# Performance work log

Hardware: AMD Instinct MI355X
Metric: run time of the kernel (lower is better)

## Reference

```python
import jax, jax.numpy as jnp
import numpy as np

E, H, D = 512, 8, 64
B, T = 2, 1024
HD = H * D


def _linear(x, W, b):
    return x @ W + b


def _ln(x, g, b):
    mu = x.mean(-1, keepdims=True)
    var = ((x - mu) ** 2).mean(-1, keepdims=True)
    return (x - mu) / jnp.sqrt(var + 1e-5) * g + b


def _l2norm(x):
    n = jnp.sqrt((x * x).sum(-1, keepdims=True))
    return x / jnp.maximum(n, 1e-12)


def setup_inputs() -> dict:
    key = jax.random.key(0)
    ks = jax.random.split(key, 32)
    s = 0.02
    inp = {
        'x': jax.random.normal(ks[0], (B, T, E), jnp.float32),
        'b_min': jax.random.normal(ks[1], (B, T, E), jnp.float32),
        'b_max': jax.random.normal(ks[2], (B, T, E), jnp.float32),
        'motif_context': jax.random.normal(ks[3], (B, T, E), jnp.float32),
        'Wk': jax.random.normal(ks[4], (E, HD), jnp.float32) * s,
        'bk': jnp.zeros((HD,), jnp.float32),
        'Wq': jax.random.normal(ks[5], (E, HD), jnp.float32) * s,
        'bq': jnp.zeros((HD,), jnp.float32),
        'Wv': jax.random.normal(ks[6], (E, HD), jnp.float32) * s,
        'bv': jnp.zeros((HD,), jnp.float32),
        'Wo': jax.random.normal(ks[7], (HD, E), jnp.float32) * s,
        'bo': jnp.zeros((E,), jnp.float32),
        'Wd': jax.random.normal(ks[8], (E, H), jnp.float32) * s,
        'bd': jnp.zeros((H,), jnp.float32),
        'Wgw': jax.random.normal(ks[9], (E, H), jnp.float32) * s,
        'bgw': jnp.zeros((H,), jnp.float32),
        'Wgf': jax.random.normal(ks[10], (E, H), jnp.float32) * s,
        'bgf': jnp.zeros((H,), jnp.float32),
        'Wps': jax.random.normal(ks[11], (E, E), jnp.float32) * s,
        'bps': jnp.zeros((E,), jnp.float32),
        'ln1_g': jnp.ones((E,), jnp.float32),
        'ln1_b': jnp.zeros((E,), jnp.float32),
        'ln2_g': jnp.ones((E,), jnp.float32),
        'ln2_b': jnp.zeros((E,), jnp.float32),
        'W1': jax.random.normal(ks[12], (E, 4 * E), jnp.float32) * s,
        'b1': jnp.zeros((4 * E,), jnp.float32),
        'W2': jax.random.normal(ks[13], (4 * E, E), jnp.float32) * s,
        'b2': jnp.zeros((E,), jnp.float32),
    }
    return inp


def reference(x, b_min, b_max, motif_context,
              Wk, bk, Wq, bq, Wv, bv, Wo, bo, Wd, bd,
              Wgw, bgw, Wgf, bgf, Wps, bps,
              ln1_g, ln1_b, ln2_g, ln2_b, W1, b1, W2, b2):
    Bs, Ts, Es = x.shape
    x_n = _ln(x, ln1_g, ln1_b)
    k = _l2norm(_linear(x_n, Wk, bk).reshape(Bs, Ts, H, D))
    q = _l2norm(_linear(x_n, Wq, bq).reshape(Bs, Ts, H, D))
    v = jnp.tanh(_linear(x_n, Wv, bv).reshape(Bs, Ts, H, D))
    d = jax.nn.softplus(_linear(x_n, Wd, bd))            # (B,T,H)
    gw = jax.nn.sigmoid(_linear(x_n, Wgw, bgw)) ** 2     # (B,T,H)
    gf = 1.0 - jax.nn.sigmoid(_linear(x_n, Wgf, bgf)) ** 2

    # gated linear recurrent scan via cumsum of rank-1 updates
    v_gated = v * (d * gw)[..., None]                    # (B,T,H,D)
    updates = jnp.einsum('bthi,bthj->bthij', v_gated, k)  # (B,T,H,D,D)
    decay = jnp.clip(d * gf, 1e-6, 0.999)
    log_decay = jnp.log(decay)[..., None, None]          # (B,T,H,1,1)
    exp_cum_decay = jnp.exp(jnp.cumsum(log_decay, axis=1))
    state = jnp.cumsum(updates / (exp_cum_decay + 1e-8), axis=1) * exp_cum_decay
    readout = jnp.einsum('bthij,bthj->bthi', state, q)   # (B,T,H,D)
    next_mem = state[:, -1]

    x2 = x + _linear(readout.reshape(Bs, Ts, HD), Wo, bo) + 0.1 * motif_context
    h = _ln(x2, ln2_g, ln2_b)
    x3 = x2 + _linear(jax.nn.gelu(_linear(h, W1, b1), approximate=False), W2, b2)
    probe = _linear(x3, Wps, bps)
    return (x3, next_mem, b_min + probe, b_max + probe)
```

## Files before the change

### kernel.cpp

```cpp
#include <hip/hip_runtime.h>


typedef unsigned short u16;
typedef unsigned int u32;
typedef __attribute__((ext_vector_type(8))) short short8;
typedef __attribute__((ext_vector_type(4))) float floatx4;

__device__ __forceinline__ float b2f(u16 u) {
  u32 x = ((u32)u) << 16;
  return __uint_as_float(x);
}
__device__ __forceinline__ u16 f2b(float f) {
  u32 x = __float_as_uint(f);
  u32 r = (x + 0x7fffu + ((x >> 16) & 1u)) >> 16;
  return (u16)r;
}
__device__ __forceinline__ float4 b4_to_f4(uint2 u) {
  float4 r;
  r.x = __uint_as_float((u.x & 0xffffu) << 16);
  r.y = __uint_as_float(u.x & 0xffff0000u);
  r.z = __uint_as_float((u.y & 0xffffu) << 16);
  r.w = __uint_as_float(u.y & 0xffff0000u);
  return r;
}

__device__ __forceinline__ void stage16(const u16* g, u16* lds_wave_base) {
  __builtin_amdgcn_global_load_lds((const __attribute__((address_space(1))) void*)g,
                                   (__attribute__((address_space(3))) void*)lds_wave_base,
                                   16, 0, 0);
}

template <int ROWS>
__device__ __forceinline__ void stage_tile(const u16* __restrict__ G, int ldK, int kb,
                                           u16* lds, int tid) {
#pragma unroll
  for (int r = 0; r < ROWS / 64; ++r) {
    int slot = r * 256 + tid;
    int row = slot >> 2;
    int kwg = (slot & 3) ^ ((row >> 1) & 3);
    stage16(G + (size_t)row * ldK + kb * 32 + kwg * 8,
            lds + (size_t)(r * 256 + (tid >> 6) * 64) * 8);
  }
}

__device__ __forceinline__ void ln_row(const float* __restrict__ xr,
                                       const float* __restrict__ g,
                                       const float* __restrict__ bt,
                                       u16* __restrict__ yr, int tid, float* red) {
  float x0 = xr[tid], x1 = xr[tid + 256];
  float s = x0 + x1, ss = x0 * x0 + x1 * x1;
#pragma unroll
  for (int o = 32; o > 0; o >>= 1) { s += __shfl_xor(s, o); ss += __shfl_xor(ss, o); }
  if ((tid & 63) == 0) { red[tid >> 6] = s; red[4 + (tid >> 6)] = ss; }
  __syncthreads();
  float ts = red[0] + red[1] + red[2] + red[3];
  float tss = red[4] + red[5] + red[6] + red[7];
  float mu = ts * (1.f / 512.f);
  float var = tss * (1.f / 512.f) - mu * mu;
  float rstd = 1.0f / sqrtf(var + 1e-5f);
  yr[tid] = f2b((x0 - mu) * rstd * g[tid] + bt[tid]);
  yr[tid + 256] = f2b((x1 - mu) * rstd * g[tid + 256] + bt[tid + 256]);
}

__global__ __launch_bounds__(256) void prep_weights(
    const float* __restrict__ Wk, const float* __restrict__ Wq,
    const float* __restrict__ Wv, const float* __restrict__ Wo,
    const float* __restrict__ Wps, const float* __restrict__ W1,
    const float* __restrict__ W2, const float* __restrict__ Wd,
    const float* __restrict__ Wgw, const float* __restrict__ Wgf,
    const float* __restrict__ bk, const float* __restrict__ bq,
    const float* __restrict__ bv, const float* __restrict__ bd,
    const float* __restrict__ bgw, const float* __restrict__ bgf,
    const float* __restrict__ x, const float* __restrict__ ln1g,
    const float* __restrict__ ln1b,
    u16* __restrict__ WTQ, u16* __restrict__ WTO, u16* __restrict__ WTPS,
    u16* __restrict__ WT1, u16* __restrict__ WT2, float* __restrict__ BQV,
    u16* __restrict__ XN) {
  int bid = blockIdx.x, tid = threadIdx.x;
  __shared__ float tile[32][33];
  __shared__ float red[8];
  if (bid < 3328) {
    const float* src;
    u16* dst;
    int C, rel, tiles_x;
    if (bid < 256)       { src = Wk;  dst = WTQ;           C = 512;  rel = bid;        tiles_x = 16; }
    else if (bid < 512)  { src = Wq;  dst = WTQ + 262144;  C = 512;  rel = bid - 256;  tiles_x = 16; }
    else if (bid < 768)  { src = Wv;  dst = WTQ + 524288;  C = 512;  rel = bid - 512;  tiles_x = 16; }
    else if (bid < 1024) { src = Wo;  dst = WTO;           C = 512;  rel = bid - 768;  tiles_x = 16; }
    else if (bid < 1280) { src = Wps; dst = WTPS;          C = 512;  rel = bid - 1024; tiles_x = 16; }
    else if (bid < 2304) { src = W1;  dst = WT1;           C = 2048; rel = bid - 1280; tiles_x = 64; }
    else                 { src = W2;  dst = WT2;           C = 512;  rel = bid - 2304; tiles_x = 16; }
    int R = (bid >= 1280 && bid < 2304) ? 512 : (bid >= 2304 ? 2048 : 512);
    int c0 = (rel % tiles_x) * 32, r0 = (rel / tiles_x) * 32;
    int tx = tid & 31, ty = tid >> 5;
#pragma unroll
    for (int i = 0; i < 4; ++i)
      tile[ty + i * 8][tx] = src[(size_t)(r0 + ty + i * 8) * C + c0 + tx];
    __syncthreads();
#pragma unroll
    for (int i = 0; i < 4; ++i)
      dst[(size_t)(c0 + ty + i * 8) * R + r0 + tx] = f2b(tile[tx][ty + i * 8]);
  } else if (bid < 3392) {
    int idx = (bid - 3328) * 256 + tid;
    const int stride = 64 * 256;
    for (int i = idx; i < 128 * 512; i += stride) {
      int local = i >> 9, k = i & 511;
      float v = 0.f;
      if (local < 8) v = Wd[k * 8 + local];
      else if (local < 16) v = Wgw[k * 8 + (local - 8)];
      else if (local < 24) v = Wgf[k * 8 + (local - 16)];
      WTQ[(size_t)(1536 + local) * 512 + k] = f2b(v);
    }
    for (int i = idx; i < 1664; i += stride) {
      float v = 0.f;
      if (i < 512) v = bk[i];
      else if (i < 1024) v = bq[i - 512];
      else if (i < 1536) v = bv[i - 1024];
      else if (i < 1544) v = bd[i - 1536];
      else if (i < 1552) v = bgw[i - 1544];
      else if (i < 1560) v = bgf[i - 1552];
      BQV[i] = v;
    }
  } else {
    int row = bid - 3392;
    ln_row(x + (size_t)row * 512, ln1g, ln1b, XN + (size_t)row * 512, tid, red);
  }
}

__global__ __launch_bounds__(256) void ln_f32(const float* __restrict__ X,
                                              const float* __restrict__ g,
                                              const float* __restrict__ bt,
                                              u16* __restrict__ Y) {
  __shared__ float red[8];
  ln_row(X + (size_t)blockIdx.x * 512, g, bt, Y + (size_t)blockIdx.x * 512,
         threadIdx.x, red);
}

template <int EPI>
__global__ __launch_bounds__(256, 4) void gemm64(
    const u16* __restrict__ A, const u16* __restrict__ BT, const float* __restrict__ bias,
    float* __restrict__ outf, float* __restrict__ outf2, u16* __restrict__ outb,
    const float* __restrict__ aux0, const float* __restrict__ aux1, int M, int N, int K) {
  __shared__ __align__(16) u16 As[3][64 * 32];
  __shared__ __align__(16) u16 Bs[3][64 * 32];
  const int tid = threadIdx.x;
  const int lane = tid & 63, wave = tid >> 6;
  const int wm = wave >> 1, wn = wave & 1;
  const int m0 = blockIdx.y * 64, n0 = blockIdx.x * 64;
  floatx4 acc[2][2] = {};
  const int fr = lane & 15, kq = lane >> 4;
  const int nk = K >> 5;
  const u16* Ab = A + (size_t)m0 * K;
  const u16* Bb = BT + (size_t)n0 * K;

  stage_tile<64>(Ab, K, 0, As[0], tid);
  stage_tile<64>(Bb, K, 0, Bs[0], tid);
  if (nk > 1) {
    stage_tile<64>(Ab, K, 1, As[1], tid);
    stage_tile<64>(Bb, K, 1, Bs[1], tid);
  }

  for (int kb = 0; kb < nk; ++kb) {
    const int cur = kb % 3;
    if (kb + 2 < nk) {
      const int nxt = (kb + 2) % 3;
      stage_tile<64>(Ab, K, kb + 2, As[nxt], tid);
      stage_tile<64>(Bb, K, kb + 2, Bs[nxt], tid);
    }
    int ahead = nk - 1 - kb;
    if (ahead > 2) ahead = 2;
    if (ahead == 2) asm volatile("s_waitcnt vmcnt(4)" ::: "memory");
    else if (ahead == 1) asm volatile("s_waitcnt vmcnt(2)" ::: "memory");
    else asm volatile("s_waitcnt vmcnt(0)" ::: "memory");
    asm volatile("s_barrier" ::: "memory");

    short8 af[2], bf[2];
#pragma unroll
    for (int mt = 0; mt < 2; ++mt) {
      int row = wm * 32 + mt * 16 + fr;
      af[mt] = *(const short8*)&As[cur][row * 32 + (kq ^ ((row >> 1) & 3)) * 8];
    }
#pragma unroll
    for (int nt = 0; nt < 2; ++nt) {
      int row = wn * 32 + nt * 16 + fr;
      bf[nt] = *(const short8*)&Bs[cur][row * 32 + (kq ^ ((row >> 1) & 3)) * 8];
    }
#pragma unroll
    for (int mt = 0; mt < 2; ++mt)
#pragma unroll
      for (int nt = 0; nt < 2; ++nt)
        acc[mt][nt] =
            __builtin_amdgcn_mfma_f32_16x16x32_bf16(af[mt], bf[nt], acc[mt][nt], 0, 0, 0);
    asm volatile("s_waitcnt lgkmcnt(0)" ::: "memory");
    asm volatile("s_barrier" ::: "memory");
  }

  const int col = lane & 15;
  const int rbase = (lane >> 4) * 4;
#pragma unroll
  for (int nt = 0; nt < 2; ++nt) {
    int gc = n0 + wn * 32 + nt * 16 + col;
    float bvv = bias[gc];
#pragma unroll
    for (int mt = 0; mt < 2; ++mt) {
      int gr = m0 + wm * 32 + mt * 16 + rbase;
#pragma unroll
      for (int r = 0; r < 4; ++r) {
        size_t idx = (size_t)(gr + r) * N + gc;
        float v = acc[mt][nt][r] + bvv;
        if constexpr (EPI == 0) {
          outf[idx] = v;
        } else if constexpr (EPI == 1) {
          outf[idx] = aux0[idx] + v + 0.1f * aux1[idx];
        } else if constexpr (EPI == 2) {
          outb[idx] = f2b(0.5f * v * (1.f + erff(v * 0.70710678118654752f)));
        } else if constexpr (EPI == 3) {
          float w = aux0[idx] + v;
          outf[idx] = w;
          outb[idx] = f2b(w);
        } else {
          outf[idx] = aux0[idx] + v;
          outf2[idx] = aux1[idx] + v;
        }
      }
    }
  }
}

__global__ __launch_bounds__(512) void post_qkvg(const float* __restrict__ C0,
                                                 u16* __restrict__ KB, u16* __restrict__ QB,
                                                 u16* __restrict__ VG,
                                                 float* __restrict__ DEC) {
  int tok = blockIdx.x;
  int b = tok >> 10, t = tok & 1023;
  int tid = threadIdx.x;
  int h = tid >> 6, d = tid & 63;
  const float* row = C0 + (size_t)tok * 1664;

  float dl = row[1536 + h], gwl = row[1544 + h], gfl = row[1552 + h];
  float dd = dl > 20.f ? dl : log1pf(expf(dl));
  float sw = 1.f / (1.f + expf(-gwl));
  float gw = sw * sw;
  float sf = 1.f / (1.f + expf(-gfl));
  float gf = 1.f - sf * sf;

  size_t obase = ((size_t)(b * 8 + h) * 1024 + t) * 64 + d;

  float kx = row[h * 64 + d];
  float ssk = kx * kx;
#pragma unroll
  for (int o = 32; o > 0; o >>= 1) ssk += __shfl_xor(ssk, o);
  KB[obase] = f2b(kx / fmaxf(sqrtf(ssk), 1e-12f));

  float qx = row[512 + h * 64 + d];
  float ssq = qx * qx;
#pragma unroll
  for (int o = 32; o > 0; o >>= 1) ssq += __shfl_xor(ssq, o);
  QB[obase] = f2b(qx / fmaxf(sqrtf(ssq), 1e-12f));

  float vx = tanhf(row[1024 + h * 64 + d]);
  VG[obase] = f2b(vx * (dd * gw));

  if (d == 0)
    DEC[(size_t)(b * 8 + h) * 1024 + t] = fminf(fmaxf(dd * gf, 1e-6f), 0.999f);
}

__global__ void logcum(const float* __restrict__ DEC, float* __restrict__ LC,
                       float* __restrict__ WW) {
  int bh = blockIdx.x;
  int lane = threadIdx.x;
  size_t base = (size_t)bh * 1024 + lane * 16;
  float loc[16];
  float run = 0.f;
#pragma unroll
  for (int i = 0; i < 16; ++i) { run += logf(DEC[base + i]); loc[i] = run; }
  float x = run;
#pragma unroll
  for (int o = 1; o < 64; o <<= 1) {
    float v = __shfl_up(x, o);
    if (lane >= o) x += v;
  }
  float excl = x - run;
#pragma unroll
  for (int i = 0; i < 16; ++i) {
    float L = excl + loc[i];
    LC[base + i] = L;
    float c = expf(L);
    WW[base + i] = c / (c + 1e-8f);
  }
}

__global__ __launch_bounds__(256, 2) void scan_phase1(
    const u16* __restrict__ KB, const u16* __restrict__ QB, const u16* __restrict__ VG,
    const float* __restrict__ DEC, const float* __restrict__ WW,
    float* __restrict__ RP, float* __restrict__ SF) {
  int chunk = blockIdx.x, h = blockIdx.y, b = blockIdx.z;
  int bh = b * 8 + h;
  int t0 = chunk * 64;
  __shared__ __align__(16) float sk[4096], sq[4096], sv[4096];
  __shared__ float lsa[64], lsw[64];
  int tid = threadIdx.x, lane = tid & 63, wave = tid >> 6;

  const u16* gk = KB + ((size_t)bh * 1024 + t0) * 64;
  const u16* gq = QB + ((size_t)bh * 1024 + t0) * 64;
  const u16* gv = VG + ((size_t)bh * 1024 + t0) * 64;
#pragma unroll
  for (int r = 0; r < 4; ++r) {
    int f = ((wave * 4 + r) * 64 + lane) * 4;
    *(float4*)&sk[f] = b4_to_f4(*(const uint2*)(gk + f));
    *(float4*)&sq[f] = b4_to_f4(*(const uint2*)(gq + f));
    *(float4*)&sv[f] = b4_to_f4(*(const uint2*)(gv + f));
  }
  if (tid < 64) {
    lsa[tid] = DEC[(size_t)bh * 1024 + t0 + tid];
    lsw[tid] = WW[(size_t)bh * 1024 + t0 + tid];
  }
  __syncthreads();

  int i = tid >> 2, j0 = (tid & 3) * 16;
  float s[16];
#pragma unroll
  for (int z = 0; z < 16; ++z) s[z] = 0.f;

  for (int t = 0; t < 64; ++t) {
    float a = lsa[t], w = lsw[t];
    float wv = w * sv[t * 64 + i];
    float r = 0.f;
#pragma unroll
    for (int u4 = 0; u4 < 4; ++u4) {
      float4 kv = *(const float4*)&sk[t * 64 + j0 + u4 * 4];
      float4 qv = *(const float4*)&sq[t * 64 + j0 + u4 * 4];
      s[u4 * 4 + 0] = fmaf(a, s[u4 * 4 + 0], wv * kv.x); r = fmaf(s[u4 * 4 + 0], qv.x, r);
      s[u4 * 4 + 1] = fmaf(a, s[u4 * 4 + 1], wv * kv.y); r = fmaf(s[u4 * 4 + 1], qv.y, r);
      s[u4 * 4 + 2] = fmaf(a, s[u4 * 4 + 2], wv * kv.z); r = fmaf(s[u4 * 4 + 2], qv.z, r);
      s[u4 * 4 + 3] = fmaf(a, s[u4 * 4 + 3], wv * kv.w); r = fmaf(s[u4 * 4 + 3], qv.w, r);
    }
    r += __shfl_xor(r, 1);
    r += __shfl_xor(r, 2);
    if ((tid & 3) == 0)
      RP[((size_t)(b * 1024 + t0 + t) * 8 + h) * 64 + i] = r;
  }

  float* Sf = SF + ((size_t)bh * 16 + chunk) * 4096 + i * 64 + j0;
#pragma unroll
  for (int u4 = 0; u4 < 4; ++u4) {
    float4 v;
    v.x = s[u4 * 4 + 0]; v.y = s[u4 * 4 + 1]; v.z = s[u4 * 4 + 2]; v.w = s[u4 * 4 + 3];
    *(float4*)&Sf[u4 * 4] = v;
  }
}

__global__ __launch_bounds__(256) void scan_phase2p(const float* __restrict__ SF,
                                                    const float* __restrict__ LC,
                                                    float* __restrict__ SI,
                                                    float* __restrict__ next_mem) {
  int bh = blockIdx.x >> 4;
  int e = (blockIdx.x & 15) * 256 + threadIdx.x;
  float s = 0.f;
  for (int c = 0; c < 16; ++c) {
    SI[((size_t)bh * 16 + c) * 4096 + e] = s;
    float Lend = LC[(size_t)bh * 1024 + c * 64 + 63];
    float Lpre = c ? LC[(size_t)bh * 1024 + c * 64 - 1] : 0.f;
    float P = expf(Lend - Lpre);
    s = fmaf(P, s, SF[((size_t)bh * 16 + c) * 4096 + e]);
  }
  next_mem[(size_t)bh * 4096 + e] = s;
}

__global__ __launch_bounds__(256, 2) void scan_phase3(
    const u16* __restrict__ QB, const float* __restrict__ SI, const float* __restrict__ LC,
    const float* __restrict__ RP, u16* __restrict__ AB) {
  int chunk = blockIdx.x, h = blockIdx.y, b = blockIdx.z;
  int bh = b * 8 + h;
  int t0 = chunk * 64;
  __shared__ __align__(16) float sq[4096];
  __shared__ float sL[64];
  int tid = threadIdx.x, lane = tid & 63, wave = tid >> 6;

  const u16* gq = QB + ((size_t)bh * 1024 + t0) * 64;
#pragma unroll
  for (int r = 0; r < 4; ++r) {
    int f = ((wave * 4 + r) * 64 + lane) * 4;
    *(float4*)&sq[f] = b4_to_f4(*(const uint2*)(gq + f));
  }
  if (tid < 64) sL[tid] = LC[(size_t)bh * 1024 + t0 + tid];
  __syncthreads();

  float Lpre = chunk ? LC[(size_t)bh * 1024 + t0 - 1] : 0.f;
  int i = tid >> 2, j0 = (tid & 3) * 16;
  const float* Si = SI + ((size_t)bh * 16 + chunk) * 4096 + i * 64 + j0;
  float S[16];
#pragma unroll
  for (int u4 = 0; u4 < 4; ++u4) {
    float4 v = *(const float4*)&Si[u4 * 4];
    S[u4 * 4 + 0] = v.x; S[u4 * 4 + 1] = v.y; S[u4 * 4 + 2] = v.z; S[u4 * 4 + 3] = v.w;
  }

  for (int t = 0; t < 64; ++t) {
    float p = expf(sL[t] - Lpre);
    float r = 0.f;
#pragma unroll
    for (int u4 = 0; u4 < 4; ++u4) {
      float4 qv = *(const float4*)&sq[t * 64 + j0 + u4 * 4];
      r = fmaf(S[u4 * 4 + 0], qv.x, r);
      r = fmaf(S[u4 * 4 + 1], qv.y, r);
      r = fmaf(S[u4 * 4 + 2], qv.z, r);
      r = fmaf(S[u4 * 4 + 3], qv.w, r);
    }
    r += __shfl_xor(r, 1);
    r += __shfl_xor(r, 2);
    if ((tid & 3) == 0) {
      size_t gi = ((size_t)(b * 1024 + t0 + t) * 8 + h) * 64 + i;
      AB[gi] = f2b(RP[gi] + p * r);
    }
  }
}

extern "C" void kernel_launch(void* const* d_in, const int* in_sizes, int n_in,
                              void* d_out, int out_size, void* d_ws, size_t ws_size,
                              hipStream_t stream) {
  const float* x = (const float*)d_in[0];
  const float* bmin = (const float*)d_in[1];
  const float* bmax = (const float*)d_in[2];
  const float* motif = (const float*)d_in[3];
  const float* Wk = (const float*)d_in[4];
  const float* bk = (const float*)d_in[5];
  const float* Wq = (const float*)d_in[6];
  const float* bq = (const float*)d_in[7];
  const float* Wv = (const float*)d_in[8];
  const float* bv = (const float*)d_in[9];
  const float* Wo = (const float*)d_in[10];
  const float* bo = (const float*)d_in[11];
  const float* Wd = (const float*)d_in[12];
  const float* bd = (const float*)d_in[13];
  const float* Wgw = (const float*)d_in[14];
  const float* bgw = (const float*)d_in[15];
  const float* Wgf = (const float*)d_in[16];
  const float* bgf = (const float*)d_in[17];
  const float* Wps = (const float*)d_in[18];
  const float* bps = (const float*)d_in[19];
  const float* ln1g = (const float*)d_in[20];
  const float* ln1b = (const float*)d_in[21];
  const float* ln2g = (const float*)d_in[22];
  const float* ln2b = (const float*)d_in[23];
  const float* W1 = (const float*)d_in[24];
  const float* b1 = (const float*)d_in[25];
  const float* W2 = (const float*)d_in[26];
  const float* b2 = (const float*)d_in[27];

  char* ws = (char*)d_ws;
  u16* WTQ = (u16*)(ws + 0);
  u16* WTO = (u16*)(ws + 1703936);
  u16* WT1 = (u16*)(ws + 2228224);
  u16* WT2 = (u16*)(ws + 4325376);
  u16* WTPS = (u16*)(ws + 6422528);
  float* BQV = (float*)(ws + 6946816);
  u16* XN = (u16*)(ws + 6953984);
  float* C0 = (float*)(ws + 9051136);
  u16* KB = (u16*)(ws + 25828352);
  u16* QB = (u16*)(ws + 27925504);
  u16* VG = (u16*)(ws + 30022656);
  float* DEC = (float*)(ws + 32119808);
  float* LC = (float*)(ws + 32185344);
  float* WW = (float*)(ws + 32250880);
  float* RP = (float*)(ws + 32316416);
  float* SF = (float*)(ws + 36510720);
  float* SI = (float*)(ws + 40705024);
  u16* AB = (u16*)(ws + 9051136);
  float* X2 = (float*)(ws + 11148288);
  u16* HB = (u16*)(ws + 15342592);
  u16* MID = (u16*)(ws + 17439744);
  u16* X3B = (u16*)(ws + 25828352);

  float* out0 = (float*)d_out;
  float* out1 = out0 + 1048576;
  float* out2 = out0 + 1114112;
  float* out3 = out0 + 2162688;

  prep_weights<<<5440, 256, 0, stream>>>(Wk, Wq, Wv, Wo, Wps, W1, W2, Wd, Wgw, Wgf,
                                         bk, bq, bv, bd, bgw, bgf, x, ln1g, ln1b,
                                         WTQ, WTO, WTPS, WT1, WT2, BQV, XN);
  gemm64<0><<<dim3(26, 32), 256, 0, stream>>>(XN, WTQ, BQV, C0, nullptr, nullptr,
                                              nullptr, nullptr, 2048, 1664, 512);
  post_qkvg<<<2048, 512, 0, stream>>>(C0, KB, QB, VG, DEC);
  logcum<<<16, 64, 0, stream>>>(DEC, LC, WW);
  scan_phase1<<<dim3(16, 8, 2), 256, 0, stream>>>(KB, QB, VG, DEC, WW, RP, SF);
  scan_phase2p<<<256, 256, 0, stream>>>(SF, LC, SI, out1);
  scan_phase3<<<dim3(16, 8, 2), 256, 0, stream>>>(QB, SI, LC, RP, AB);

  gemm64<1><<<dim3(8, 32), 256, 0, stream>>>(AB, WTO, bo, X2, nullptr, nullptr,
                                             x, motif, 2048, 512, 512);
  ln_f32<<<2048, 256, 0, stream>>>(X2, ln2g, ln2b, HB);
  gemm64<2><<<dim3(32, 32), 256, 0, stream>>>(HB, WT1, b1, nullptr, nullptr, MID,
                                              nullptr, nullptr, 2048, 2048, 512);
  gemm64<3><<<dim3(8, 32), 256, 0, stream>>>(MID, WT2, b2, out0, nullptr, X3B,
                                             X2, nullptr, 2048, 512, 2048);
  gemm64<4><<<dim3(8, 32), 256, 0, stream>>>(X3B, WTPS, bps, out2, out3, nullptr,
                                             bmin, bmax, 2048, 512, 512);
}
```

Measured before the change: 264.0 us.

## Deepen GEMM K-tile to 64 and use 32-row tiles for narrow-N GEMMs

The shared GEMM kernel now stages 64-wide K slices per pipeline step instead of 32, with a wider 8-way XOR swizzle. That halves the number of barrier and waitcnt rounds per K loop. It is also templated on the M tile size, and the three N=512 GEMMs switch to 32-row tiles, which doubles their block count (512 blocks) so the GPU's CUs are better filled. In exchange LDS per block grows, occupancy hints change, and the vmcnt thresholds had to be retuned for the new per-stage load counts.

```diff
diff --git a/kernel.cpp b/kernel.cpp
--- a/kernel.cpp
+++ b/kernel.cpp
@@ -31,14 +31,14 @@
 }
 
 template <int ROWS>
-__device__ __forceinline__ void stage_tile(const u16* __restrict__ G, int ldK, int kb,
-                                           u16* lds, int tid) {
-#pragma unroll
-  for (int r = 0; r < ROWS / 64; ++r) {
+__device__ __forceinline__ void stage_tile64(const u16* __restrict__ G, int ldK, int kb,
+                                             u16* lds, int tid) {
+#pragma unroll
+  for (int r = 0; r < ROWS / 32; ++r) {
     int slot = r * 256 + tid;
-    int row = slot >> 2;
-    int kwg = (slot & 3) ^ ((row >> 1) & 3);
-    stage16(G + (size_t)row * ldK + kb * 32 + kwg * 8,
+    int row = slot >> 3;
+    int kwg = (slot & 7) ^ (row & 7);
+    stage16(G + (size_t)row * ldK + kb * 64 + kwg * 8,
             lds + (size_t)(r * 256 + (tid >> 6) * 64) * 8);
   }
 }
@@ -136,61 +136,74 @@
          threadIdx.x, red);
 }
 
-template <int EPI>
-__global__ __launch_bounds__(256, 4) void gemm64(
+template <int BM, int EPI>
+__global__ __launch_bounds__(256, (BM == 64 ? 3 : 4)) void gemm64k(
     const u16* __restrict__ A, const u16* __restrict__ BT, const float* __restrict__ bias,
     float* __restrict__ outf, float* __restrict__ outf2, u16* __restrict__ outb,
     const float* __restrict__ aux0, const float* __restrict__ aux1, int M, int N, int K) {
-  __shared__ __align__(16) u16 As[3][64 * 32];
-  __shared__ __align__(16) u16 Bs[3][64 * 32];
+  constexpr int MT = BM / 32;
+  constexpr int S = BM / 32 + 2;
+  __shared__ __align__(16) u16 As[3][BM * 64];
+  __shared__ __align__(16) u16 Bs[3][64 * 64];
   const int tid = threadIdx.x;
   const int lane = tid & 63, wave = tid >> 6;
   const int wm = wave >> 1, wn = wave & 1;
-  const int m0 = blockIdx.y * 64, n0 = blockIdx.x * 64;
-  floatx4 acc[2][2] = {};
+  const int m0 = blockIdx.y * BM, n0 = blockIdx.x * 64;
+  floatx4 acc[MT][2] = {};
   const int fr = lane & 15, kq = lane >> 4;
-  const int nk = K >> 5;
+  const int nk = K >> 6;
   const u16* Ab = A + (size_t)m0 * K;
   const u16* Bb = BT + (size_t)n0 * K;
 
-  stage_tile<64>(Ab, K, 0, As[0], tid);
-  stage_tile<64>(Bb, K, 0, Bs[0], tid);
+  stage_tile64<BM>(Ab, K, 0, As[0], tid);
+  stage_tile64<64>(Bb, K, 0, Bs[0], tid);
   if (nk > 1) {
-    stage_tile<64>(Ab, K, 1, As[1], tid);
-    stage_tile<64>(Bb, K, 1, Bs[1], tid);
+    stage_tile64<BM>(Ab, K, 1, As[1], tid);
+    stage_tile64<64>(Bb, K, 1, Bs[1], tid);
   }
 
   for (int kb = 0; kb < nk; ++kb) {
     const int cur = kb % 3;
     if (kb + 2 < nk) {
       const int nxt = (kb + 2) % 3;
-      stage_tile<64>(Ab, K, kb + 2, As[nxt], tid);
-      stage_tile<64>(Bb, K, kb + 2, Bs[nxt], tid);
+      stage_tile64<BM>(Ab, K, kb + 2, As[nxt], tid);
+      stage_tile64<64>(Bb, K, kb + 2, Bs[nxt], tid);
     }
     int ahead = nk - 1 - kb;
     if (ahead > 2) ahead = 2;
-    if (ahead == 2) asm volatile("s_waitcnt vmcnt(4)" ::: "memory");
-    else if (ahead == 1) asm volatile("s_waitcnt vmcnt(2)" ::: "memory");
-    else asm volatile("s_waitcnt vmcnt(0)" ::: "memory");
+    if (ahead == 2) {
+      if constexpr (S == 4) asm volatile("s_waitcnt vmcnt(8)" ::: "memory");
+      else asm volatile("s_waitcnt vmcnt(6)" ::: "memory");
+    } else if (ahead == 1) {
+      if constexpr (S == 4) asm volatile("s_waitcnt vmcnt(4)" ::: "memory");
+      else asm volatile("s_waitcnt vmcnt(3)" ::: "memory");
+    } else {
+      asm volatile("s_waitcnt vmcnt(0)" ::: "memory");
+    }
     asm volatile("s_barrier" ::: "memory");
 
-    short8 af[2], bf[2];
-#pragma unroll
-    for (int mt = 0; mt < 2; ++mt) {
-      int row = wm * 32 + mt * 16 + fr;
-      af[mt] = *(const short8*)&As[cur][row * 32 + (kq ^ ((row >> 1) & 3)) * 8];
-    }
-#pragma unroll
-    for (int nt = 0; nt < 2; ++nt) {
-      int row = wn * 32 + nt * 16 + fr;
-      bf[nt] = *(const short8*)&Bs[cur][row * 32 + (kq ^ ((row >> 1) & 3)) * 8];
-    }
-#pragma unroll
-    for (int mt = 0; mt < 2; ++mt)
-#pragma unroll
-      for (int nt = 0; nt < 2; ++nt)
-        acc[mt][nt] =
-            __builtin_amdgcn_mfma_f32_16x16x32_bf16(af[mt], bf[nt], acc[mt][nt], 0, 0, 0);
+#pragma unroll
+    for (int sub = 0; sub < 2; ++sub) {
+      short8 af[MT], bf[2];
+#pragma unroll
+      for (int mt = 0; mt < MT; ++mt) {
+        int row = wm * (BM / 2) + mt * 16 + fr;
+        int c = sub * 4 + kq;
+        af[mt] = *(const short8*)&As[cur][row * 64 + ((c ^ (row & 7)) << 3)];
+      }
+#pragma unroll
+      for (int nt = 0; nt < 2; ++nt) {
+        int row = wn * 32 + nt * 16 + fr;
+        int c = sub * 4 + kq;
+        bf[nt] = *(const short8*)&Bs[cur][row * 64 + ((c ^ (row & 7)) << 3)];
+      }
+#pragma unroll
+      for (int mt = 0; mt < MT; ++mt)
+#pragma unroll
+        for (int nt = 0; nt < 2; ++nt)
+          acc[mt][nt] =
+              __builtin_amdgcn_mfma_f32_16x16x32_bf16(af[mt], bf[nt], acc[mt][nt], 0, 0, 0);
+    }
     asm volatile("s_waitcnt lgkmcnt(0)" ::: "memory");
     asm volatile("s_barrier" ::: "memory");
   }
@@ -202,8 +215,8 @@
     int gc = n0 + wn * 32 + nt * 16 + col;
     float bvv = bias[gc];
 #pragma unroll
-    for (int mt = 0; mt < 2; ++mt) {
-      int gr = m0 + wm * 32 + mt * 16 + rbase;
+    for (int mt = 0; mt < MT; ++mt) {
+      int gr = m0 + wm * (BM / 2) + mt * 16 + rbase;
 #pragma unroll
       for (int r = 0; r < 4; ++r) {
         size_t idx = (size_t)(gr + r) * N + gc;
@@ -480,21 +493,21 @@
   prep_weights<<<5440, 256, 0, stream>>>(Wk, Wq, Wv, Wo, Wps, W1, W2, Wd, Wgw, Wgf,
                                          bk, bq, bv, bd, bgw, bgf, x, ln1g, ln1b,
                                          WTQ, WTO, WTPS, WT1, WT2, BQV, XN);
-  gemm64<0><<<dim3(26, 32), 256, 0, stream>>>(XN, WTQ, BQV, C0, nullptr, nullptr,
-                                              nullptr, nullptr, 2048, 1664, 512);
+  gemm64k<64, 0><<<dim3(26, 32), 256, 0, stream>>>(XN, WTQ, BQV, C0, nullptr, nullptr,
+                                                   nullptr, nullptr, 2048, 1664, 512);
   post_qkvg<<<2048, 512, 0, stream>>>(C0, KB, QB, VG, DEC);
   logcum<<<16, 64, 0, stream>>>(DEC, LC, WW);
   scan_phase1<<<dim3(16, 8, 2), 256, 0, stream>>>(KB, QB, VG, DEC, WW, RP, SF);
   scan_phase2p<<<256, 256, 0, stream>>>(SF, LC, SI, out1);
   scan_phase3<<<dim3(16, 8, 2), 256, 0, stream>>>(QB, SI, LC, RP, AB);
 
-  gemm64<1><<<dim3(8, 32), 256, 0, stream>>>(AB, WTO, bo, X2, nullptr, nullptr,
-                                             x, motif, 2048, 512, 512);
+  gemm64k<32, 1><<<dim3(8, 64), 256, 0, stream>>>(AB, WTO, bo, X2, nullptr, nullptr,
+                                                  x, motif, 2048, 512, 512);
   ln_f32<<<2048, 256, 0, stream>>>(X2, ln2g, ln2b, HB);
-  gemm64<2><<<dim3(32, 32), 256, 0, stream>>>(HB, WT1, b1, nullptr, nullptr, MID,
-                                              nullptr, nullptr, 2048, 2048, 512);
-  gemm64<3><<<dim3(8, 32), 256, 0, stream>>>(MID, WT2, b2, out0, nullptr, X3B,
-                                             X2, nullptr, 2048, 512, 2048);
-  gemm64<4><<<dim3(8, 32), 256, 0, stream>>>(X3B, WTPS, bps, out2, out3, nullptr,
-                                             bmin, bmax, 2048, 512, 512);
-}
+  gemm64k<64, 2><<<dim3(32, 32), 256, 0, stream>>>(HB, WT1, b1, nullptr, nullptr, MID,
+                                                   nullptr, nullptr, 2048, 2048, 512);
+  gemm64k<32, 3><<<dim3(8, 64), 256, 0, stream>>>(MID, WT2, b2, out0, nullptr, X3B,
+                                                  X2, nullptr, 2048, 512, 2048);
+  gemm64k<32, 4><<<dim3(8, 64), 256, 0, stream>>>(X3B, WTPS, bps, out2, out3, nullptr,
+                                                  bmin, bmax, 2048, 512, 512);
+}
```

Measured after the change: 258.7 us. -2.0%, faster.
